# Kernel optimization log

Hardware: AMD Instinct MI355X
Metric: run time of the kernel (lower is better)

Reference implementation:

```python
import jax, jax.numpy as jnp
import numpy as np

INF = jnp.float32(jnp.inf)
# 8 grid directions (the torch module always uses all 8; self.diagonal is never read)
DIRS = jnp.array([[-1, 0], [1, 0], [0, -1], [0, 1],
                  [-1, -1], [-1, 1], [1, -1], [1, 1]], dtype=jnp.int32)


def setup_inputs() -> dict:
    key = jax.random.key(0)
    b, n = 128, 32
    weights = jax.random.uniform(key, (b, n, n), dtype=jnp.float32)
    return {"weights": weights}


def _dijkstra_path(weights):
    b, n, _ = weights.shape
    ar = jnp.arange(b)

    dist = jnp.full((b, n, n), INF, dtype=weights.dtype).at[:, 0, 0].set(0.0)
    vis = jnp.zeros((b, n, n), dtype=bool)
    pred = jnp.zeros((b, n, n, 2), dtype=jnp.int32)

    def relax_step(_, state):
        dist, vis, pred = state
        # pick unvisited node with minimum distance, per batch element
        unvis = jnp.where(vis, INF, dist)                       # (b, n, n)
        idx = jnp.argmin(unvis.reshape(b, -1), axis=1)          # (b,)
        cy, cx = idx // n, idx % n
        vis = vis.at[ar, cy, cx].set(True)
        cur = dist[ar, cy, cx]                                   # (b,)

        # 8 neighbors, vectorized over the direction axis
        ny = cy[:, None] + DIRS[None, :, 0]                      # (b, 8)
        nx = cx[:, None] + DIRS[None, :, 1]
        valid = (ny >= 0) & (ny < n) & (nx >= 0) & (nx < n)
        nyc = jnp.clip(ny, 0, n - 1)
        nxc = jnp.clip(nx, 0, n - 1)
        bb = jnp.broadcast_to(ar[:, None], (b, 8))

        old = dist[bb, nyc, nxc]
        nvis = vis[bb, nyc, nxc]
        new = cur[:, None] + weights[bb, nyc, nxc]
        upd = valid & ~nvis & (new < old)

        # duplicate-safe relaxation: scatter-min with inf where no update
        dist = dist.at[bb, nyc, nxc].min(jnp.where(upd, new, INF))
        # cells updated this step all get predecessor (cy, cx)
        umask = jnp.zeros((b, n, n), dtype=bool).at[bb, nyc, nxc].max(upd)
        cur_yx = jnp.stack([cy, cx], axis=-1)[:, None, None, :]  # (b,1,1,2)
        pred = jnp.where(umask[..., None], cur_yx.astype(pred.dtype), pred)
        return dist, vis, pred

    # Running the full n*n relaxations is equivalent to the torch early-break:
    # by Dijkstra's invariant, the target's distance/predecessor are final once
    # it would be popped, and later pops never alter the target path.
    dist, vis, pred = jax.lax.fori_loop(0, n * n, relax_step, (dist, vis, pred))

    # backtrack from (n-1, n-1) to (0, 0); pred[0,0] == (0,0) so it is a fixed point
    path = jnp.zeros((b, n, n), dtype=jnp.float32).at[:, n - 1, n - 1].set(1.0)

    def back_step(_, state):
        path, cy, cx = state
        py = pred[ar, cy, cx, 0]
        px = pred[ar, cy, cx, 1]
        path = path.at[ar, py, px].set(1.0)
        return path, py, px

    start = jnp.full((b,), n - 1, dtype=jnp.int32)
    path, _, _ = jax.lax.fori_loop(0, n * n, back_step, (path, start, start))
    return path


def reference(weights) -> jnp.ndarray:
    return _dijkstra_path(weights)
```

## Files before the change

kernel.cpp:

```cpp
#include <hip/hip_runtime.h>

#define N   32
#define NN  1024
#define PS  34
#define PSZ (PS * PS)

__global__ __launch_bounds__(64, 1) void dijkstra_path_kernel(
    const float* __restrict__ weights, float* __restrict__ out)
{
    const int b    = blockIdx.x;
    const int lane = threadIdx.x & 63;
    const int ty   = lane >> 3;
    const int tx   = lane & 7;
    const int y0   = ty << 2;
    const int x0   = tx << 2;

    __shared__ float dist[PSZ];
    __shared__ int   pred[NN];
    __shared__ float pathf[NN];

    const float INF = __builtin_huge_valf();

    #pragma unroll
    for (int k = 0; k < 19; ++k) {
        int idx = lane + k * 64;
        if (idx < PSZ) dist[idx] = INF;
    }
    #pragma unroll
    for (int k = 0; k < 16; ++k) pathf[lane + k * 64] = 0.0f;

    float w[4][4];
    const float* wb = weights + b * NN;
    #pragma unroll
    for (int i = 0; i < 4; ++i) {
        const float4 v = *(const float4*)(wb + (y0 + i) * N + x0);
        w[i][0] = v.x; w[i][1] = v.y; w[i][2] = v.z; w[i][3] = v.w;
    }

    float g[6][6];
    #pragma unroll
    for (int i = 0; i < 6; ++i)
        #pragma unroll
        for (int j = 0; j < 6; ++j) g[i][j] = INF;
    if (lane == 0) {
        g[1][1] = 0.0f;
        dist[1 * PS + 1] = 0.0f;
    }
    __threadfence_block();

#define RELAX(i, j)                                                           \
    {                                                                         \
        const float m = fminf(                                                \
            fminf(fminf(g[(i)-1][(j)-1], g[(i)-1][(j)]),                      \
                  fminf(g[(i)-1][(j)+1], g[(i)][(j)-1])),                     \
            fminf(fminf(g[(i)][(j)+1], g[(i)+1][(j)-1]),                      \
                  fminf(g[(i)+1][(j)], g[(i)+1][(j)+1])));                    \
        const float nv = m + w[(i)-1][(j)-1];                                 \
        if (nv < g[(i)][(j)]) { g[(i)][(j)] = nv; changed = true; }           \
    }

    const int base_top = y0 * PS + x0;
    const int base_bot = (y0 + 5) * PS + x0;
    for (int it = 0; it < 256; ++it) {
        {
            const float4 a = *(const float4*)&dist[base_top];
            g[0][0] = a.x; g[0][1] = a.y; g[0][2] = a.z; g[0][3] = a.w;
            const float2 c = *(const float2*)&dist[base_top + 4];
            g[0][4] = c.x; g[0][5] = c.y;
        }
        {
            const float4 a = *(const float4*)&dist[base_bot - 2];
            const float4 c = *(const float4*)&dist[base_bot + 2];
            g[5][0] = a.z; g[5][1] = a.w;
            g[5][2] = c.x; g[5][3] = c.y; g[5][4] = c.z; g[5][5] = c.w;
        }
        #pragma unroll
        for (int i = 0; i < 4; ++i) {
            const int r = (y0 + i + 1) * PS + x0;
            g[1 + i][0] = dist[r];
            g[1 + i][5] = dist[r + 5];
        }

        bool changed = false;
        #pragma unroll
        for (int i = 1; i <= 4; ++i)
            #pragma unroll
            for (int j = 1; j <= 4; ++j) RELAX(i, j)
        #pragma unroll
        for (int i = 4; i >= 1; --i)
            #pragma unroll
            for (int j = 1; j <= 4; ++j) RELAX(i, j)
        #pragma unroll
        for (int i = 1; i <= 4; ++i)
            #pragma unroll
            for (int j = 4; j >= 1; --j) RELAX(i, j)
        #pragma unroll
        for (int i = 4; i >= 1; --i)
            #pragma unroll
            for (int j = 4; j >= 1; --j) RELAX(i, j)

        #pragma unroll
        for (int i = 0; i < 4; ++i) {
            const int r = (y0 + i + 1) * PS + (x0 + 1);
            dist[r]     = g[1 + i][1];
            dist[r + 1] = g[1 + i][2];
            dist[r + 2] = g[1 + i][3];
            dist[r + 3] = g[1 + i][4];
        }
        __threadfence_block();
        if (!__any((int)changed)) break;
    }
#undef RELAX

    const int dy[8] = {-1, 1, 0, 0, -1, -1, 1, 1};
    const int dx[8] = { 0, 0,-1, 1, -1,  1,-1, 1};
    #pragma unroll
    for (int i = 0; i < 4; ++i)
        #pragma unroll
        for (int j = 0; j < 4; ++j) {
            const int yy = y0 + i, xx = x0 + j;
            const int t  = yy * N + xx;
            int p = 0;
            if (t != 0) {
                float best = INF;
                #pragma unroll
                for (int k = 0; k < 8; ++k) {
                    const float u = g[1 + i + dy[k]][1 + j + dx[k]];
                    const float c = u + w[i][j];
                    if (c < best) { best = c; p = (yy + dy[k]) * N + (xx + dx[k]); }
                }
            }
            pred[t] = p;
        }
    __threadfence_block();

    if (lane == 0) {
        int cur = NN - 1;
        pathf[cur] = 1.0f;
        for (int s = 0; s < NN && cur != 0; ++s) {
            cur = pred[cur];
            pathf[cur] = 1.0f;
        }
    }
    __threadfence_block();

    float* ob = out + b * NN;
    #pragma unroll
    for (int i = 0; i < 4; ++i) {
        const int t = (y0 + i) * N + x0;
        const float4 v = *(const float4*)&pathf[t];
        *(float4*)(ob + t) = v;
    }
}

extern "C" void kernel_launch(void* const* d_in, const int* in_sizes, int n_in,
                              void* d_out, int out_size, void* d_ws, size_t ws_size,
                              hipStream_t stream) {
    const float* w = (const float*)d_in[0];
    float* out = (float*)d_out;
    const int b = in_sizes[0] / NN;
    dijkstra_path_kernel<<<dim3(b), dim3(64), 0, stream>>>(w, out);
}
```

Before: 87.34 us.

## Exchange tile halos via wavefront shuffles and cut relaxation sweeps to two

Drops the padded shared-memory distance grid. Each thread now gets its 4x4 tile's halo from neighbouring lanes with __shfl, and boundary tiles are masked to INF, which removes the LDS stores and loads plus the fences on every iteration. The per-iteration sweeps also go from four directions to two (forward and reverse). That lowers work per iteration but may need more outer iterations before convergence.

```diff
diff --git a/kernel.cpp b/kernel.cpp
--- a/kernel.cpp
+++ b/kernel.cpp
@@ -2,8 +2,6 @@
 
 #define N   32
 #define NN  1024
-#define PS  34
-#define PSZ (PS * PS)
 
 __global__ __launch_bounds__(64, 1) void dijkstra_path_kernel(
     const float* __restrict__ weights, float* __restrict__ out)
@@ -15,17 +13,11 @@
     const int y0   = ty << 2;
     const int x0   = tx << 2;
 
-    __shared__ float dist[PSZ];
     __shared__ int   pred[NN];
     __shared__ float pathf[NN];
 
     const float INF = __builtin_huge_valf();
 
-    #pragma unroll
-    for (int k = 0; k < 19; ++k) {
-        int idx = lane + k * 64;
-        if (idx < PSZ) dist[idx] = INF;
-    }
     #pragma unroll
     for (int k = 0; k < 16; ++k) pathf[lane + k * 64] = 0.0f;
 
@@ -42,11 +34,9 @@
     for (int i = 0; i < 6; ++i)
         #pragma unroll
         for (int j = 0; j < 6; ++j) g[i][j] = INF;
-    if (lane == 0) {
-        g[1][1] = 0.0f;
-        dist[1 * PS + 1] = 0.0f;
-    }
-    __threadfence_block();
+    if (lane == 0) g[1][1] = 0.0f;
+
+    const bool hT = (ty > 0), hB = (ty < 7), hL = (tx > 0), hR = (tx < 7);
 
 #define RELAX(i, j)                                                           \
     {                                                                         \
@@ -59,27 +49,35 @@
         if (nv < g[(i)][(j)]) { g[(i)][(j)] = nv; changed = true; }           \
     }
 
-    const int base_top = y0 * PS + x0;
-    const int base_bot = (y0 + 5) * PS + x0;
     for (int it = 0; it < 256; ++it) {
-        {
-            const float4 a = *(const float4*)&dist[base_top];
-            g[0][0] = a.x; g[0][1] = a.y; g[0][2] = a.z; g[0][3] = a.w;
-            const float2 c = *(const float2*)&dist[base_top + 4];
-            g[0][4] = c.x; g[0][5] = c.y;
-        }
-        {
-            const float4 a = *(const float4*)&dist[base_bot - 2];
-            const float4 c = *(const float4*)&dist[base_bot + 2];
-            g[5][0] = a.z; g[5][1] = a.w;
-            g[5][2] = c.x; g[5][3] = c.y; g[5][4] = c.z; g[5][5] = c.w;
+        float tT[4], tB[4], tL[4], tR[4];
+        #pragma unroll
+        for (int j = 0; j < 4; ++j) tT[j] = __shfl(g[4][1 + j], lane - 8);
+        #pragma unroll
+        for (int j = 0; j < 4; ++j) tB[j] = __shfl(g[1][1 + j], lane + 8);
+        #pragma unroll
+        for (int i = 0; i < 4; ++i) tL[i] = __shfl(g[1 + i][4], lane - 1);
+        #pragma unroll
+        for (int i = 0; i < 4; ++i) tR[i] = __shfl(g[1 + i][1], lane + 1);
+        const float cTL = __shfl(g[4][4], lane - 9);
+        const float cTR = __shfl(g[4][1], lane - 7);
+        const float cBL = __shfl(g[1][4], lane + 7);
+        const float cBR = __shfl(g[1][1], lane + 9);
+
+        #pragma unroll
+        for (int j = 0; j < 4; ++j) {
+            g[0][1 + j] = hT ? tT[j] : INF;
+            g[5][1 + j] = hB ? tB[j] : INF;
         }
         #pragma unroll
         for (int i = 0; i < 4; ++i) {
-            const int r = (y0 + i + 1) * PS + x0;
-            g[1 + i][0] = dist[r];
-            g[1 + i][5] = dist[r + 5];
+            g[1 + i][0] = hL ? tL[i] : INF;
+            g[1 + i][5] = hR ? tR[i] : INF;
         }
+        g[0][0] = (hT && hL) ? cTL : INF;
+        g[0][5] = (hT && hR) ? cTR : INF;
+        g[5][0] = (hB && hL) ? cBL : INF;
+        g[5][5] = (hB && hR) ? cBR : INF;
 
         bool changed = false;
         #pragma unroll
@@ -89,25 +87,8 @@
         #pragma unroll
         for (int i = 4; i >= 1; --i)
             #pragma unroll
-            for (int j = 1; j <= 4; ++j) RELAX(i, j)
-        #pragma unroll
-        for (int i = 1; i <= 4; ++i)
-            #pragma unroll
-            for (int j = 4; j >= 1; --j) RELAX(i, j)
-        #pragma unroll
-        for (int i = 4; i >= 1; --i)
-            #pragma unroll
             for (int j = 4; j >= 1; --j) RELAX(i, j)
 
-        #pragma unroll
-        for (int i = 0; i < 4; ++i) {
-            const int r = (y0 + i + 1) * PS + (x0 + 1);
-            dist[r]     = g[1 + i][1];
-            dist[r + 1] = g[1 + i][2];
-            dist[r + 2] = g[1 + i][3];
-            dist[r + 3] = g[1 + i][4];
-        }
-        __threadfence_block();
         if (!__any((int)changed)) break;
     }
 #undef RELAX
```

New measurement: 74.58 us. -14.6%, faster.
